# Optimization experiments

Measured on AMD Instinct MI355X. Metric: run time of the kernel, lower is better.

The kernel has to match this reference:

```python
import jax, jax.numpy as jnp
import numpy as np

B, L, E = 2, 2048, 1024
H, DKV = 16, 64


def setup_inputs() -> dict:
    key = jax.random.key(0)
    k1, k2 = jax.random.split(key)
    X = jax.random.normal(k1, (B, L, E), dtype=jnp.float32)
    # nn.Linear(embed_dim, n_heads*3*d_kv): weight stored here as [in, out]
    W_qkv = jax.random.normal(k2, (E, 3 * H * DKV), dtype=jnp.float32) * (1.0 / np.sqrt(E))
    b_qkv = jnp.zeros((3 * H * DKV,), dtype=jnp.float32)
    return {"X": X, "W_qkv": W_qkv, "b_qkv": b_qkv}


def reference(X, W_qkv, b_qkv):
    b, l, _ = X.shape
    # fused QKV projection, then 'b l (h 3*dkv)' -> [b, l, h, 3*dkv] -> chunk(3)
    qkv = (X @ W_qkv + b_qkv).reshape(b, l, H, 3 * DKV)
    Q, K, V = jnp.split(qkv, 3, axis=-1)  # each [b, l, h, dkv]
    # attn_scores: einsum('bkhd, blhd -> bhkl') / sqrt(d_kv)
    scores = jnp.einsum('bkhd,blhd->bhkl', Q, K) / np.sqrt(DKV).astype(np.float32)
    # attn_mask defaults to None -> no causal masking applied
    attn_weights = jax.nn.softmax(scores, axis=-1)  # [b, h, l, l]
    return attn_weights
```

## Files before the change

kernel.cpp:

```cpp
#include <hip/hip_runtime.h>
#include <hip/hip_bf16.h>

typedef _Float16 half4v __attribute__((ext_vector_type(4)));
typedef _Float16 half8v __attribute__((ext_vector_type(8)));
typedef float float4v __attribute__((ext_vector_type(4)));
typedef float float16v __attribute__((ext_vector_type(16)));

#define L_SEQ 2048
#define EMB 1024
#define NH 16
#define DKV 64

__device__ inline void gll16(const void* g, void* l) {
  __builtin_amdgcn_global_load_lds((const __attribute__((address_space(1))) void*)g,
                                   (__attribute__((address_space(3))) void*)l, 16, 0, 0);
}

__global__ __launch_bounds__(256) void xcast_kernel(const float* __restrict__ X,
                                                    _Float16* __restrict__ X16) {
  size_t i = ((size_t)blockIdx.x * 256 + threadIdx.x) * 8;
  float4v v0 = *(const float4v*)(X + i);
  float4v v1 = *(const float4v*)(X + i + 4);
  half8v h;
  h[0] = (_Float16)v0[0]; h[1] = (_Float16)v0[1]; h[2] = (_Float16)v0[2]; h[3] = (_Float16)v0[3];
  h[4] = (_Float16)v1[0]; h[5] = (_Float16)v1[1]; h[6] = (_Float16)v1[2]; h[7] = (_Float16)v1[3];
  *(half8v*)(X16 + i) = h;
}

__global__ __launch_bounds__(256) void wpack_kernel(const float* __restrict__ W,
                                                    _Float16* __restrict__ Wt) {
  __shared__ float tile[32][33];
  int n0 = blockIdx.x * 32;
  int k0 = blockIdx.y * 32;
  int h = n0 >> 7;
  int wc = h * 192 + (n0 & 127);
  int tx = threadIdx.x & 31;
  int ty = threadIdx.x >> 5;
#pragma unroll
  for (int i = 0; i < 4; ++i) {
    int k = ty + i * 8;
    tile[k][tx] = W[(size_t)(k0 + k) * 3072 + wc + tx];
  }
  __syncthreads();
#pragma unroll
  for (int i = 0; i < 4; ++i) {
    int n = ty + i * 8;
    Wt[(size_t)(n0 + n) * 1024 + k0 + tx] = (_Float16)tile[tx][n];
  }
}

__global__ __launch_bounds__(256) void qk_gemm_kernel(const _Float16* __restrict__ X16,
                                                      const _Float16* __restrict__ Wt,
                                                      const float* __restrict__ bias,
                                                      _Float16* __restrict__ Qh,
                                                      _Float16* __restrict__ Kh) {
  __shared__ _Float16 As[128 * 32];
  __shared__ _Float16 Bs[128 * 32];
  int n0 = blockIdx.x * 128;
  int m0 = blockIdx.y * 128;
  int t = threadIdx.x;
  int l = t & 63;
  int wv = t >> 6;
  int wm = wv >> 1, wn = wv & 1;
  int cl = l & 15, ko = (l >> 4) * 8;
  int srow = (l >> 2);
  int scol = (l & 3) * 8;
  float4v acc[4][4] = {};
  for (int k0 = 0; k0 < 1024; k0 += 32) {
#pragma unroll
    for (int c = 0; c < 2; ++c) {
      int rbase = wv * 32 + c * 16;
      gll16(X16 + (size_t)(m0 + rbase + srow) * 1024 + k0 + scol, &As[rbase * 32]);
      gll16(Wt + (size_t)(n0 + rbase + srow) * 1024 + k0 + scol, &Bs[rbase * 32]);
    }
    __syncthreads();
    half8v a[4], b[4];
#pragma unroll
    for (int mt = 0; mt < 4; ++mt) a[mt] = *(const half8v*)(&As[(wm * 64 + mt * 16 + cl) * 32 + ko]);
#pragma unroll
    for (int nt = 0; nt < 4; ++nt) b[nt] = *(const half8v*)(&Bs[(wn * 64 + nt * 16 + cl) * 32 + ko]);
#pragma unroll
    for (int mt = 0; mt < 4; ++mt)
#pragma unroll
      for (int nt = 0; nt < 4; ++nt)
        acc[mt][nt] = __builtin_amdgcn_mfma_f32_16x16x32_f16(a[mt], b[nt], acc[mt][nt], 0, 0, 0);
    __syncthreads();
  }
#pragma unroll
  for (int mt = 0; mt < 4; ++mt) {
#pragma unroll
    for (int nt = 0; nt < 4; ++nt) {
      int n_g = n0 + wn * 64 + nt * 16 + cl;
      int hh = n_g >> 7, rr = n_g & 127;
      float bv = bias[hh * 192 + rr];
      _Float16* dstbase = (rr < 64) ? Qh : Kh;
      int d = rr & 63;
#pragma unroll
      for (int r = 0; r < 4; ++r) {
        int row_g = m0 + wm * 64 + mt * 16 + (l >> 4) * 4 + r;
        int bb = row_g >> 11, lr = row_g & 2047;
        dstbase[(((size_t)bb * NH + hh) * L_SEQ + lr) * DKV + d] = (_Float16)(acc[mt][nt][r] + bv);
      }
    }
  }
}

__global__ __launch_bounds__(256, 4) void attn_softmax_kernel(const _Float16* __restrict__ Qh,
                                                              const _Float16* __restrict__ Kh,
                                                              float* __restrict__ out) {
  __shared__ _Float16 Ks[2][128 * 64];
  __shared__ float sums[4][32];
  int id = blockIdx.x;
  int xcd = id & 7;
  int rest = id >> 3;
  int rb = rest & 31;
  int bh = ((rest >> 5) << 3) + xcd;
  int t = threadIdx.x;
  int l = t & 63;
  int wv = t >> 6;
  int lj = l & 31;
  int hk = l >> 5;
  int qh = wv & 1;
  int jh = wv >> 1;
  int qbase = rb * 64;
  const _Float16* Qb = Qh + ((size_t)bh * L_SEQ + qbase) * DKV;
  const _Float16* Kb = Kh + (size_t)bh * L_SEQ * DKV;
  const float SC = 0.18033688011112042f;

  half8v bq[4];
#pragma unroll
  for (int ks = 0; ks < 4; ++ks)
    bq[ks] = *(const half8v*)(Qb + (size_t)(qh * 32 + lj) * DKV + ks * 16 + hk * 8);

#define STAGE(bufi, j0)                                                     \
  {                                                                         \
    _Pragma("unroll") for (int c = 0; c < 4; ++c) {                         \
      int gi = (wv * 4 + c) * 64 + l;                                       \
      int r_ = gi >> 3, s_ = gi & 7;                                        \
      gll16(Kb + (size_t)((j0) + r_) * DKV + 8 * (s_ ^ (r_ & 7)),           \
            &Ks[bufi][(wv * 4 + c) * 512]);                                 \
    }                                                                       \
  }

  float lsum = 0.f;
  int buf = 0;
  STAGE(0, 0);
  __syncthreads();
  for (int s = 0; s < 16; ++s) {
    if (s + 1 < 16) STAGE(buf ^ 1, (s + 1) * 128);
#pragma unroll
    for (int q2 = 0; q2 < 2; ++q2) {
      int jq = jh * 2 + q2;
      int krow = jq * 32 + lj;
      half8v bk[4];
#pragma unroll
      for (int ks = 0; ks < 4; ++ks)
        bk[ks] = *(const half8v*)(&Ks[buf][krow * 64 + 8 * ((2 * ks + hk) ^ (krow & 7))]);
      float16v acc = {};
#pragma unroll
      for (int ks = 0; ks < 4; ++ks)
        acc = __builtin_amdgcn_mfma_f32_32x32x16_f16(bk[ks], bq[ks], acc, 0, 0, 0);
#pragma unroll
      for (int i = 0; i < 16; ++i) lsum += __builtin_amdgcn_exp2f(acc[i] * SC);
    }
    __syncthreads();
    buf ^= 1;
  }
  lsum += __shfl_xor(lsum, 32);
  if (l < 32) sums[wv][lj] = lsum;
  __syncthreads();

  float cc[16];
#pragma unroll
  for (int i = 0; i < 16; ++i) {
    int qo = (i & 3) + 8 * (i >> 2) + 4 * hk;
    cc[i] = -__log2f(sums[qh][qo] + sums[qh + 2][qo]);
  }

  size_t orow0 = ((size_t)bh * L_SEQ + qbase + qh * 32) * L_SEQ;
  STAGE(0, 0);
  __syncthreads();
  buf = 0;
  for (int s = 0; s < 16; ++s) {
    if (s + 1 < 16) STAGE(buf ^ 1, (s + 1) * 128);
#pragma unroll
    for (int q2 = 0; q2 < 2; ++q2) {
      int jq = jh * 2 + q2;
      int krow = jq * 32 + lj;
      half8v bk[4];
#pragma unroll
      for (int ks = 0; ks < 4; ++ks)
        bk[ks] = *(const half8v*)(&Ks[buf][krow * 64 + 8 * ((2 * ks + hk) ^ (krow & 7))]);
      float16v acc = {};
#pragma unroll
      for (int ks = 0; ks < 4; ++ks)
        acc = __builtin_amdgcn_mfma_f32_32x32x16_f16(bq[ks], bk[ks], acc, 0, 0, 0);
      size_t col = (size_t)s * 128 + jq * 32 + lj;
#pragma unroll
      for (int i = 0; i < 16; ++i) {
        float p = __builtin_amdgcn_exp2f(acc[i] * SC + cc[i]);
        int qo = (i & 3) + 8 * (i >> 2) + 4 * hk;
        __builtin_nontemporal_store(p, out + orow0 + (size_t)qo * L_SEQ + col);
      }
    }
    __syncthreads();
    buf ^= 1;
  }
#undef STAGE
}

extern "C" void kernel_launch(void* const* d_in, const int* in_sizes, int n_in,
                              void* d_out, int out_size, void* d_ws, size_t ws_size,
                              hipStream_t stream) {
  const float* X = (const float*)d_in[0];
  const float* W = (const float*)d_in[1];
  const float* bias = (const float*)d_in[2];
  float* out = (float*)d_out;
  char* ws = (char*)d_ws;
  _Float16* Wt = (_Float16*)ws;
  _Float16* Qh = (_Float16*)(ws + (4ull << 20));
  _Float16* Kh = (_Float16*)(ws + (12ull << 20));
  _Float16* X16 = (_Float16*)(ws + (20ull << 20));

  xcast_kernel<<<2048, 256, 0, stream>>>(X, X16);
  wpack_kernel<<<dim3(64, 32), 256, 0, stream>>>(W, Wt);
  qk_gemm_kernel<<<dim3(16, 32), 256, 0, stream>>>(X16, Wt, bias, Qh, Kh);
  attn_softmax_kernel<<<1024, 256, 0, stream>>>(Qh, Kh, out);
}
```

Before: 162.8 us.

## Interleave second query half's row-sum pass with first half's output pass

```diff
diff --git a/kernel.cpp b/kernel.cpp
--- a/kernel.cpp
+++ b/kernel.cpp
@@ -109,28 +109,30 @@
                                                               const _Float16* __restrict__ Kh,
                                                               float* __restrict__ out) {
   __shared__ _Float16 Ks[2][128 * 64];
-  __shared__ float sums[4][32];
+  __shared__ float red[4][32];
+  __shared__ float ccs[2][32];
   int id = blockIdx.x;
   int xcd = id & 7;
   int rest = id >> 3;
-  int rb = rest & 31;
+  int pr = rest & 31;
   int bh = ((rest >> 5) << 3) + xcd;
   int t = threadIdx.x;
   int l = t & 63;
   int wv = t >> 6;
   int lj = l & 31;
   int hk = l >> 5;
-  int qh = wv & 1;
-  int jh = wv >> 1;
-  int qbase = rb * 64;
-  const _Float16* Qb = Qh + ((size_t)bh * L_SEQ + qbase) * DKV;
+  int qA = pr * 64, qB = pr * 64 + 32;
+  const _Float16* Qb = Qh + (size_t)bh * L_SEQ * DKV;
   const _Float16* Kb = Kh + (size_t)bh * L_SEQ * DKV;
   const float SC = 0.18033688011112042f;
 
-  half8v bq[4];
-#pragma unroll
-  for (int ks = 0; ks < 4; ++ks)
-    bq[ks] = *(const half8v*)(Qb + (size_t)(qh * 32 + lj) * DKV + ks * 16 + hk * 8);
+  half8v bqA[4], bqB[4];
+#pragma unroll
+  for (int ks = 0; ks < 4; ++ks) {
+    bqA[ks] = *(const half8v*)(Qb + (size_t)(qA + lj) * DKV + ks * 16 + hk * 8);
+    bqB[ks] = *(const half8v*)(Qb + (size_t)(qB + lj) * DKV + ks * 16 + hk * 8);
+  }
+  int krow = wv * 32 + lj;
 
 #define STAGE(bufi, j0)                                                     \
   {                                                                         \
@@ -141,72 +143,87 @@
             &Ks[bufi][(wv * 4 + c) * 512]);                                 \
     }                                                                       \
   }
-
-  float lsum = 0.f;
+#define LOADBK(bk, bufi)                                                    \
+  _Pragma("unroll") for (int ks = 0; ks < 4; ++ks)                          \
+      bk[ks] = *(const half8v*)(&Ks[bufi][krow * 64 + 8 * ((2 * ks + hk) ^ (krow & 7))]);
+
   int buf = 0;
   STAGE(0, 0);
   __syncthreads();
+
+  float lsum = 0.f;
+  for (int s = 0; s < 16; ++s) {
+    STAGE(buf ^ 1, ((s + 1) & 15) * 128);
+    half8v bk[4];
+    LOADBK(bk, buf);
+    float16v acc = {};
+#pragma unroll
+    for (int ks = 0; ks < 4; ++ks)
+      acc = __builtin_amdgcn_mfma_f32_32x32x16_f16(bk[ks], bqA[ks], acc, 0, 0, 0);
+#pragma unroll
+    for (int i = 0; i < 16; ++i) lsum += __builtin_amdgcn_exp2f(acc[i] * SC);
+    __syncthreads();
+    buf ^= 1;
+  }
+  lsum += __shfl_xor(lsum, 32);
+  if (l < 32) red[wv][lj] = lsum;
+  __syncthreads();
+  if (t < 32) ccs[0][t] = -__log2f(red[0][t] + red[1][t] + red[2][t] + red[3][t]);
+  __syncthreads();
+
+  size_t orowA = ((size_t)bh * L_SEQ + qA) * L_SEQ;
+  lsum = 0.f;
+  for (int s = 0; s < 16; ++s) {
+    STAGE(buf ^ 1, ((s + 1) & 15) * 128);
+    half8v bk[4];
+    LOADBK(bk, buf);
+    float16v acc = {};
+#pragma unroll
+    for (int ks = 0; ks < 4; ++ks)
+      acc = __builtin_amdgcn_mfma_f32_32x32x16_f16(bqA[ks], bk[ks], acc, 0, 0, 0);
+    size_t col = (size_t)s * 128 + wv * 32 + lj;
+#pragma unroll
+    for (int i = 0; i < 16; ++i) {
+      int qo = (i & 3) + 8 * (i >> 2) + 4 * hk;
+      float p = __builtin_amdgcn_exp2f(acc[i] * SC + ccs[0][qo]);
+      __builtin_nontemporal_store(p, out + orowA + (size_t)qo * L_SEQ + col);
+    }
+    float16v acc2 = {};
+#pragma unroll
+    for (int ks = 0; ks < 4; ++ks)
+      acc2 = __builtin_amdgcn_mfma_f32_32x32x16_f16(bk[ks], bqB[ks], acc2, 0, 0, 0);
+#pragma unroll
+    for (int i = 0; i < 16; ++i) lsum += __builtin_amdgcn_exp2f(acc2[i] * SC);
+    __syncthreads();
+    buf ^= 1;
+  }
+  lsum += __shfl_xor(lsum, 32);
+  if (l < 32) red[wv][lj] = lsum;
+  __syncthreads();
+  if (t < 32) ccs[1][t] = -__log2f(red[0][t] + red[1][t] + red[2][t] + red[3][t]);
+  __syncthreads();
+
+  size_t orowB = ((size_t)bh * L_SEQ + qB) * L_SEQ;
   for (int s = 0; s < 16; ++s) {
     if (s + 1 < 16) STAGE(buf ^ 1, (s + 1) * 128);
-#pragma unroll
-    for (int q2 = 0; q2 < 2; ++q2) {
-      int jq = jh * 2 + q2;
-      int krow = jq * 32 + lj;
-      half8v bk[4];
-#pragma unroll
-      for (int ks = 0; ks < 4; ++ks)
-        bk[ks] = *(const half8v*)(&Ks[buf][krow * 64 + 8 * ((2 * ks + hk) ^ (krow & 7))]);
-      float16v acc = {};
-#pragma unroll
-      for (int ks = 0; ks < 4; ++ks)
-        acc = __builtin_amdgcn_mfma_f32_32x32x16_f16(bk[ks], bq[ks], acc, 0, 0, 0);
-#pragma unroll
-      for (int i = 0; i < 16; ++i) lsum += __builtin_amdgcn_exp2f(acc[i] * SC);
+    half8v bk[4];
+    LOADBK(bk, buf);
+    float16v acc = {};
+#pragma unroll
+    for (int ks = 0; ks < 4; ++ks)
+      acc = __builtin_amdgcn_mfma_f32_32x32x16_f16(bqB[ks], bk[ks], acc, 0, 0, 0);
+    size_t col = (size_t)s * 128 + wv * 32 + lj;
+#pragma unroll
+    for (int i = 0; i < 16; ++i) {
+      int qo = (i & 3) + 8 * (i >> 2) + 4 * hk;
+      float p = __builtin_amdgcn_exp2f(acc[i] * SC + ccs[1][qo]);
+      __builtin_nontemporal_store(p, out + orowB + (size_t)qo * L_SEQ + col);
     }
     __syncthreads();
     buf ^= 1;
   }
-  lsum += __shfl_xor(lsum, 32);
-  if (l < 32) sums[wv][lj] = lsum;
-  __syncthreads();
-
-  float cc[16];
-#pragma unroll
-  for (int i = 0; i < 16; ++i) {
-    int qo = (i & 3) + 8 * (i >> 2) + 4 * hk;
-    cc[i] = -__log2f(sums[qh][qo] + sums[qh + 2][qo]);
-  }
-
-  size_t orow0 = ((size_t)bh * L_SEQ + qbase + qh * 32) * L_SEQ;
-  STAGE(0, 0);
-  __syncthreads();
-  buf = 0;
-  for (int s = 0; s < 16; ++s) {
-    if (s + 1 < 16) STAGE(buf ^ 1, (s + 1) * 128);
-#pragma unroll
-    for (int q2 = 0; q2 < 2; ++q2) {
-      int jq = jh * 2 + q2;
-      int krow = jq * 32 + lj;
-      half8v bk[4];
-#pragma unroll
-      for (int ks = 0; ks < 4; ++ks)
-        bk[ks] = *(const half8v*)(&Ks[buf][krow * 64 + 8 * ((2 * ks + hk) ^ (krow & 7))]);
-      float16v acc = {};
-#pragma unroll
-      for (int ks = 0; ks < 4; ++ks)
-        acc = __builtin_amdgcn_mfma_f32_32x32x16_f16(bq[ks], bk[ks], acc, 0, 0, 0);
-      size_t col = (size_t)s * 128 + jq * 32 + lj;
-#pragma unroll
-      for (int i = 0; i < 16; ++i) {
-        float p = __builtin_amdgcn_exp2f(acc[i] * SC + cc[i]);
-        int qo = (i & 3) + 8 * (i >> 2) + 4 * hk;
-        __builtin_nontemporal_store(p, out + orow0 + (size_t)qo * L_SEQ + col);
-      }
-    }
-    __syncthreads();
-    buf ^= 1;
-  }
 #undef STAGE
+#undef LOADBK
 }
 
 extern "C" void kernel_launch(void* const* d_in, const int* in_sizes, int n_in,
```

New measurement: 161.6 us. Within noise of the previous version (-0.7%).
